# Optimization experiments

Hardware: AMD Instinct MI355X
Metric: run time of the kernel (lower is better)

## Reference

```python
import jax, jax.numpy as jnp
import numpy as np

D_MODEL = 1024
D_FF = 4 * D_MODEL
NUM_EXPERTS = 8
TOP_K = 2
B, L = 4, 2048


def setup_inputs() -> dict:
    key = jax.random.key(0)
    ks = jax.random.split(key, 7)
    s = 0.02
    return {
        "x": jax.random.normal(ks[0], (B, L, D_MODEL), dtype=jnp.float32),
        "Wr": jax.random.normal(ks[1], (D_MODEL, NUM_EXPERTS), dtype=jnp.float32) * s,
        "br": jnp.zeros((NUM_EXPERTS,), dtype=jnp.float32),
        "W1": jax.random.normal(ks[2], (NUM_EXPERTS, D_MODEL, D_FF), dtype=jnp.float32) * s,
        "b1": jnp.zeros((NUM_EXPERTS, D_FF), dtype=jnp.float32),
        "W2": jax.random.normal(ks[3], (NUM_EXPERTS, D_FF, D_MODEL), dtype=jnp.float32) * s,
        "b2": jnp.zeros((NUM_EXPERTS, D_MODEL), dtype=jnp.float32),
    }


def reference(x, Wr, br, W1, b1, W2, b2):
    Bb, Ll, D = x.shape
    x_flat = x.reshape(-1, D)                      # [T, D]
    T = x_flat.shape[0]

    # Router: softmax over experts, then top-k and renormalize (matches torch)
    logits = x_flat @ Wr + br                      # [T, E]
    probs = jax.nn.softmax(logits, axis=-1)
    topk_w, topk_idx = jax.lax.top_k(probs, TOP_K)  # [T, K]
    topk_w = topk_w / jnp.sum(topk_w, axis=-1, keepdims=True)

    # Per-token per-expert combine weights: w_full[t, e] = sum_k topk_w[t,k] * (topk_idx[t,k]==e)
    # (top_k indices are distinct, so scatter-add equals the masked-overwrite loop)
    w_full = jnp.zeros((T, NUM_EXPERTS), dtype=x.dtype)
    rows = jnp.arange(T)[:, None]
    w_full = w_full.at[rows, topk_idx].add(topk_w)

    # Dense all-expert MLP (same math as masked per-expert dispatch; dropout is eval/no-op)
    h = jax.nn.gelu(jnp.einsum("td,edf->etf", x_flat, W1) + b1[:, None, :], approximate=False)
    y = jnp.einsum("etf,efd->etd", h, W2) + b2[:, None, :]   # [E, T, D]
    out = jnp.einsum("te,etd->td", w_full, y)                # [T, D]
    return out.reshape(Bb, Ll, D)
```

## Files before the change

### kernel.cpp

```cpp
#include <hip/hip_runtime.h>
#include <hip/hip_bf16.h>

#define T_TOKENS 8192
#define DM 1024
#define DF 4096
#define NE 8
#define NROWS 16384

typedef __attribute__((ext_vector_type(8))) short bf16x8;
typedef __attribute__((ext_vector_type(8))) unsigned short ushort8;
typedef __attribute__((ext_vector_type(4))) float f32x4;

__device__ inline unsigned short f2bf(float f) {
  unsigned int u = __builtin_bit_cast(unsigned int, f);
  u = (u + 0x7fffu + ((u >> 16) & 1u)) >> 16;
  return (unsigned short)u;
}

__device__ inline float bf2f(unsigned short s) {
  unsigned int u = ((unsigned int)s) << 16;
  return __builtin_bit_cast(float, u);
}

__device__ __forceinline__ void gload16(const unsigned short* g, unsigned short* l) {
  __builtin_amdgcn_global_load_lds(
      (const __attribute__((address_space(1))) unsigned int*)g,
      (__attribute__((address_space(3))) unsigned int*)l,
      16, 0, 0);
}

__global__ void router_kernel(const float* __restrict__ x,
                              const float* __restrict__ Wr,
                              const float* __restrict__ br,
                              int* __restrict__ ctrl,
                              int* __restrict__ tope,
                              float* __restrict__ topw,
                              unsigned short* __restrict__ xb) {
  const int wid = threadIdx.x >> 6;
  const int lane = threadIdx.x & 63;
  const int t = blockIdx.x * 4 + wid;
  const float* xr = x + (size_t)t * DM;
  unsigned short* xbr = xb + (size_t)t * DM;
  float a[NE];
#pragma unroll
  for (int e = 0; e < NE; ++e) a[e] = 0.f;
#pragma unroll
  for (int it = 0; it < 4; ++it) {
    const int d0 = it * 256 + lane * 4;
    const float4 xv = *(const float4*)(xr + d0);
    ushort4 o;
    o.x = f2bf(xv.x); o.y = f2bf(xv.y); o.z = f2bf(xv.z); o.w = f2bf(xv.w);
    *(ushort4*)(xbr + d0) = o;
    const float xs[4] = {xv.x, xv.y, xv.z, xv.w};
#pragma unroll
    for (int j = 0; j < 4; ++j) {
      const float4 wa = *(const float4*)(Wr + (size_t)(d0 + j) * NE);
      const float4 wb = *(const float4*)(Wr + (size_t)(d0 + j) * NE + 4);
      a[0] += xs[j] * wa.x; a[1] += xs[j] * wa.y;
      a[2] += xs[j] * wa.z; a[3] += xs[j] * wa.w;
      a[4] += xs[j] * wb.x; a[5] += xs[j] * wb.y;
      a[6] += xs[j] * wb.z; a[7] += xs[j] * wb.w;
    }
  }
#pragma unroll
  for (int off = 32; off > 0; off >>= 1) {
#pragma unroll
    for (int e = 0; e < NE; ++e) a[e] += __shfl_xor(a[e], off);
  }
  if (lane == 0) {
    float lg[NE];
    float m = -1e30f;
#pragma unroll
    for (int e = 0; e < NE; ++e) { lg[e] = a[e] + br[e]; m = fmaxf(m, lg[e]); }
    float p[NE];
#pragma unroll
    for (int e = 0; e < NE; ++e) p[e] = expf(lg[e] - m);
    int i0 = 0;
#pragma unroll
    for (int e = 1; e < NE; ++e) if (p[e] > p[i0]) i0 = e;
    int i1 = (i0 == 0) ? 1 : 0;
#pragma unroll
    for (int e = 0; e < NE; ++e) if (e != i0 && p[e] > p[i1]) i1 = e;
    const float s = p[i0] + p[i1];
    tope[2 * t] = i0;
    tope[2 * t + 1] = i1;
    topw[2 * t] = p[i0] / s;
    topw[2 * t + 1] = p[i1] / s;
    atomicAdd(&ctrl[i0], 1);
    atomicAdd(&ctrl[i1], 1);
  }
}

__global__ void scan_kernel(int* __restrict__ ctrl) {
  if (threadIdx.x == 0 && blockIdx.x == 0) {
    int off = 0;
    for (int e = 0; e < NE; ++e) {
      ctrl[8 + e] = off;
      ctrl[20 + e] = off;
      off += ctrl[e];
    }
    ctrl[16] = off;
  }
}

__global__ void place_kernel(const int* __restrict__ tope,
                             const float* __restrict__ topw,
                             int* __restrict__ ctrl,
                             int* __restrict__ rowlist,
                             float* __restrict__ roww,
                             int* __restrict__ posmap) {
  const int t = blockIdx.x * blockDim.x + threadIdx.x;
#pragma unroll
  for (int k = 0; k < 2; ++k) {
    const int e = tope[2 * t + k];
    const int pos = atomicAdd(&ctrl[20 + e], 1);
    rowlist[pos] = t;
    roww[pos] = topw[2 * t + k];
    posmap[2 * t + k] = pos;
  }
}

__global__ void transpose_cvt_kernel(const float* __restrict__ in,
                                     unsigned short* __restrict__ outp,
                                     int R, int C) {
  __shared__ float tile[64][65];
  const int e = blockIdx.z;
  const int r0 = blockIdx.y * 64;
  const int c0 = blockIdx.x * 64;
  const float* src = in + ((size_t)e * R + r0) * C + c0;
  const int tid = threadIdx.x;
  const int rr0 = tid >> 4;
  const int cc4 = (tid & 15) * 4;
#pragma unroll
  for (int i = 0; i < 4; ++i) {
    const int rr = rr0 + i * 16;
    const float4 v = *(const float4*)(src + (size_t)rr * C + cc4);
    tile[rr][cc4] = v.x; tile[rr][cc4 + 1] = v.y;
    tile[rr][cc4 + 2] = v.z; tile[rr][cc4 + 3] = v.w;
  }
  __syncthreads();
  unsigned short* dst = outp + ((size_t)e * C + c0) * R + r0;
  const int orr = (tid & 7) * 8;
  const int oc0 = tid >> 3;
#pragma unroll
  for (int i = 0; i < 2; ++i) {
    const int oc = oc0 + i * 32;
    ushort8 o;
#pragma unroll
    for (int j = 0; j < 8; ++j) o[j] = f2bf(tile[orr + j][oc]);
    *(ushort8*)(dst + (size_t)oc * R + orr) = o;
  }
}

__global__ __launch_bounds__(256, 4) void gemm1_kernel(
    const unsigned short* __restrict__ xb,
    const unsigned short* __restrict__ w1t,
    const float* __restrict__ b1,
    const int* __restrict__ ctrl,
    const int* __restrict__ rowlist,
    unsigned short* __restrict__ h) {
  const int e = blockIdx.z;
  const int count = ctrl[e];
  const int mt = blockIdx.y;
  if (mt * 128 >= count) return;
  const int off = ctrl[8 + e];
  const int n0 = blockIdx.x * 128;
  const int tid = threadIdx.x;
  const int wid = tid >> 6;
  const int lane = tid & 63;
  const int wm = (wid & 1) * 64;
  const int wn = (wid >> 1) * 64;
  const int q = lane >> 4;
  const int l16 = lane & 15;
  const int rl = lane >> 3;
  const int ch = lane & 7;
  const int sch = ch ^ rl;

  __shared__ __attribute__((aligned(16))) unsigned short lA[128 * 64];
  __shared__ __attribute__((aligned(16))) unsigned short lB[128 * 64];

  const unsigned short* aBase[4];
  const unsigned short* bBase[4];
  unsigned short* lABase[4];
  unsigned short* lBBase[4];
#pragma unroll
  for (int i = 0; i < 4; ++i) {
    const int r = wid * 32 + i * 8 + rl;
    int rr = mt * 128 + r;
    if (rr >= count) rr = count - 1;
    const int tok = rowlist[off + rr];
    aBase[i] = xb + (size_t)tok * DM + sch * 8;
    bBase[i] = w1t + ((size_t)e * DF + n0 + r) * DM + sch * 8;
    lABase[i] = &lA[(wid * 32 + i * 8) * 64];
    lBBase[i] = &lB[(wid * 32 + i * 8) * 64];
  }

  f32x4 acc[4][4];
  const f32x4 z = {0.f, 0.f, 0.f, 0.f};
#pragma unroll
  for (int im = 0; im < 4; ++im)
#pragma unroll
    for (int in = 0; in < 4; ++in) acc[im][in] = z;

  for (int k0 = 0; k0 < DM; k0 += 64) {
#pragma unroll
    for (int i = 0; i < 4; ++i) gload16(aBase[i] + k0, lABase[i]);
#pragma unroll
    for (int i = 0; i < 4; ++i) gload16(bBase[i] + k0, lBBase[i]);
    __syncthreads();
#pragma unroll
    for (int ks = 0; ks < 2; ++ks) {
      const int pc = ((ks * 4 + q) ^ (l16 & 7)) * 8;
      bf16x8 af[4], bfr[4];
#pragma unroll
      for (int im = 0; im < 4; ++im)
        af[im] = *(const bf16x8*)&lA[(wm + im * 16 + l16) * 64 + pc];
#pragma unroll
      for (int in = 0; in < 4; ++in)
        bfr[in] = *(const bf16x8*)&lB[(wn + in * 16 + l16) * 64 + pc];
#pragma unroll
      for (int im = 0; im < 4; ++im)
#pragma unroll
        for (int in = 0; in < 4; ++in)
          acc[im][in] = __builtin_amdgcn_mfma_f32_16x16x32_bf16(
              bfr[in], af[im], acc[im][in], 0, 0, 0);
    }
    __syncthreads();
  }

#pragma unroll
  for (int im = 0; im < 4; ++im) {
    const int r = mt * 128 + wm + im * 16 + l16;
    if (r < count) {
      unsigned short* hrow = h + ((size_t)(off + r)) * DF + n0 + wn + q * 4;
#pragma unroll
      for (int in = 0; in < 4; ++in) {
        const float4 bv = *(const float4*)(b1 + (size_t)e * DF + n0 + wn + in * 16 + q * 4);
        float v0 = acc[im][in][0] + bv.x;
        float v1 = acc[im][in][1] + bv.y;
        float v2 = acc[im][in][2] + bv.z;
        float v3 = acc[im][in][3] + bv.w;
        ushort4 o;
        o.x = f2bf(0.5f * v0 * (1.0f + erff(v0 * 0.70710678118f)));
        o.y = f2bf(0.5f * v1 * (1.0f + erff(v1 * 0.70710678118f)));
        o.z = f2bf(0.5f * v2 * (1.0f + erff(v2 * 0.70710678118f)));
        o.w = f2bf(0.5f * v3 * (1.0f + erff(v3 * 0.70710678118f)));
        *(ushort4*)(hrow + in * 16) = o;
      }
    }
  }
}

__global__ __launch_bounds__(256, 2) void gemm2_kernel(
    const unsigned short* __restrict__ h,
    const unsigned short* __restrict__ w2t,
    const float* __restrict__ b2,
    const int* __restrict__ ctrl,
    unsigned short* __restrict__ y) {
  const int e = blockIdx.z;
  const int count = ctrl[e];
  const int mt = blockIdx.x;
  if (mt * 128 >= count) return;
  const int off = ctrl[8 + e];
  const int n0 = blockIdx.y * 256;
  const int tid = threadIdx.x;
  const int wid = tid >> 6;
  const int lane = tid & 63;
  const int wm = (wid & 1) * 64;
  const int wn = (wid >> 1) * 128;
  const int q = lane >> 4;
  const int l16 = lane & 15;
  const int rl = lane >> 3;
  const int ch = lane & 7;
  const int sch = ch ^ rl;

  __shared__ __attribute__((aligned(16))) unsigned short lA[128 * 64];
  __shared__ __attribute__((aligned(16))) unsigned short lB[256 * 64];

  const unsigned short* aBase[4];
  const unsigned short* bBase[8];
  unsigned short* lABase[4];
  unsigned short* lBBase[8];
#pragma unroll
  for (int i = 0; i < 4; ++i) {
    const int r = wid * 32 + i * 8 + rl;
    int rr = mt * 128 + r;
    if (rr >= count) rr = count - 1;
    aBase[i] = h + (size_t)(off + rr) * DF + sch * 8;
    lABase[i] = &lA[(wid * 32 + i * 8) * 64];
  }
#pragma unroll
  for (int i = 0; i < 8; ++i) {
    const int r = wid * 64 + i * 8 + rl;
    bBase[i] = w2t + ((size_t)e * DM + n0 + r) * DF + sch * 8;
    lBBase[i] = &lB[(wid * 64 + i * 8) * 64];
  }

  f32x4 acc[4][8];
  const f32x4 z = {0.f, 0.f, 0.f, 0.f};
#pragma unroll
  for (int im = 0; im < 4; ++im)
#pragma unroll
    for (int in = 0; in < 8; ++in) acc[im][in] = z;

  for (int k0 = 0; k0 < DF; k0 += 64) {
#pragma unroll
    for (int i = 0; i < 4; ++i) gload16(aBase[i] + k0, lABase[i]);
#pragma unroll
    for (int i = 0; i < 8; ++i) gload16(bBase[i] + k0, lBBase[i]);
    __syncthreads();
#pragma unroll
    for (int ks = 0; ks < 2; ++ks) {
      const int pc = ((ks * 4 + q) ^ (l16 & 7)) * 8;
      bf16x8 af[4], bfr[8];
#pragma unroll
      for (int im = 0; im < 4; ++im)
        af[im] = *(const bf16x8*)&lA[(wm + im * 16 + l16) * 64 + pc];
#pragma unroll
      for (int in = 0; in < 8; ++in)
        bfr[in] = *(const bf16x8*)&lB[(wn + in * 16 + l16) * 64 + pc];
#pragma unroll
      for (int im = 0; im < 4; ++im)
#pragma unroll
        for (int in = 0; in < 8; ++in)
          acc[im][in] = __builtin_amdgcn_mfma_f32_16x16x32_bf16(
              bfr[in], af[im], acc[im][in], 0, 0, 0);
    }
    __syncthreads();
  }

#pragma unroll
  for (int im = 0; im < 4; ++im) {
    const int r = mt * 128 + wm + im * 16 + l16;
    if (r < count) {
      unsigned short* yrow = y + ((size_t)(off + r)) * DM + n0 + wn + q * 4;
#pragma unroll
      for (int in = 0; in < 8; ++in) {
        const float4 bv = *(const float4*)(b2 + (size_t)e * DM + n0 + wn + in * 16 + q * 4);
        ushort4 o;
        o.x = f2bf(acc[im][in][0] + bv.x);
        o.y = f2bf(acc[im][in][1] + bv.y);
        o.z = f2bf(acc[im][in][2] + bv.z);
        o.w = f2bf(acc[im][in][3] + bv.w);
        *(ushort4*)(yrow + in * 16) = o;
      }
    }
  }
}

__global__ void combine_kernel(const unsigned short* __restrict__ y,
                               const int* __restrict__ posmap,
                               const float* __restrict__ topw,
                               float* __restrict__ out) {
  const int t = blockIdx.x;
  const int c = threadIdx.x * 4;
  const int p0 = posmap[2 * t];
  const int p1 = posmap[2 * t + 1];
  const float w0 = topw[2 * t];
  const float w1 = topw[2 * t + 1];
  const ushort4 a = *(const ushort4*)(y + (size_t)p0 * DM + c);
  const ushort4 b = *(const ushort4*)(y + (size_t)p1 * DM + c);
  float4 o;
  o.x = w0 * bf2f(a.x) + w1 * bf2f(b.x);
  o.y = w0 * bf2f(a.y) + w1 * bf2f(b.y);
  o.z = w0 * bf2f(a.z) + w1 * bf2f(b.z);
  o.w = w0 * bf2f(a.w) + w1 * bf2f(b.w);
  *(float4*)(out + (size_t)t * DM + c) = o;
}

extern "C" void kernel_launch(void* const* d_in, const int* in_sizes, int n_in,
                              void* d_out, int out_size, void* d_ws, size_t ws_size,
                              hipStream_t stream) {
  const float* x  = (const float*)d_in[0];
  const float* Wr = (const float*)d_in[1];
  const float* br = (const float*)d_in[2];
  const float* W1 = (const float*)d_in[3];
  const float* b1 = (const float*)d_in[4];
  const float* W2 = (const float*)d_in[5];
  const float* b2 = (const float*)d_in[6];
  float* out = (float*)d_out;

  char* p = (char*)d_ws;
  auto alloc = [&](size_t bytes) -> char* {
    char* r = p;
    p += (bytes + 255) & ~(size_t)255;
    return r;
  };
  int* ctrl = (int*)alloc(1024);
  int* tope = (int*)alloc((size_t)2 * T_TOKENS * 4);
  float* topw = (float*)alloc((size_t)2 * T_TOKENS * 4);
  int* rowlist = (int*)alloc((size_t)NROWS * 4);
  float* roww = (float*)alloc((size_t)NROWS * 4);
  int* posmap = (int*)alloc((size_t)NROWS * 4);
  unsigned short* xb  = (unsigned short*)alloc((size_t)T_TOKENS * DM * 2);
  unsigned short* w1t = (unsigned short*)alloc((size_t)NE * DF * DM * 2);
  unsigned short* w2t = (unsigned short*)alloc((size_t)NE * DM * DF * 2);
  unsigned short* h   = (unsigned short*)alloc((size_t)NROWS * DF * 2);
  if ((size_t)(p - (char*)d_ws) > ws_size) return;

  unsigned short* y = w1t;

  hipMemsetAsync(ctrl, 0, 1024, stream);

  router_kernel<<<T_TOKENS / 4, 256, 0, stream>>>(x, Wr, br, ctrl, tope, topw, xb);
  scan_kernel<<<1, 64, 0, stream>>>(ctrl);
  place_kernel<<<T_TOKENS / 256, 256, 0, stream>>>(tope, topw, ctrl, rowlist, roww, posmap);
  transpose_cvt_kernel<<<dim3(DF / 64, DM / 64, NE), 256, 0, stream>>>(W1, w1t, DM, DF);
  transpose_cvt_kernel<<<dim3(DM / 64, DF / 64, NE), 256, 0, stream>>>(W2, w2t, DF, DM);
  gemm1_kernel<<<dim3(DF / 128, 64, NE), 256, 0, stream>>>(xb, w1t, b1, ctrl, rowlist, h);
  gemm2_kernel<<<dim3(64, DM / 256, NE), 256, 0, stream>>>(h, w2t, b2, ctrl, y);
  combine_kernel<<<T_TOKENS, 256, 0, stream>>>(y, posmap, topw, out);
}
```

Baseline: 1.103 ms.

## Stage GEMM epilogues through LDS for coalesced stores; use fast erf approximation

Both GEMM epilogues now write the bf16 results into the reused shared-memory buffer with an XOR swizzle, then copy them out as full 16-byte contiguous row stores instead of scattered 8-byte fragment stores. GEMM1 also replaces erff with an Abramowitz-Stegun polynomial built on rcp and exp, and hoists the bias loads out of the row loop. This aims to cut epilogue store inefficiency and the cost of GELU, at the price of extra LDS traffic and barriers, plus a small accuracy loss in GELU.

```diff
diff --git a/kernel.cpp b/kernel.cpp
--- a/kernel.cpp
+++ b/kernel.cpp
@@ -20,6 +20,19 @@
 __device__ inline float bf2f(unsigned short s) {
   unsigned int u = ((unsigned int)s) << 16;
   return __builtin_bit_cast(float, u);
+}
+
+__device__ __forceinline__ float gelu_f(float v) {
+  const float z = fabsf(v) * 0.70710678118f;
+  const float t = __builtin_amdgcn_rcpf(1.0f + 0.3275911f * z);
+  const float poly =
+      t * (0.254829592f +
+           t * (-0.284496736f +
+                t * (1.421413741f + t * (-1.453152027f + t * 1.061405429f))));
+  const float ee = __expf(-z * z);
+  float er = 1.0f - poly * ee;
+  er = (v < 0.0f) ? -er : er;
+  return 0.5f * v * (1.0f + er);
 }
 
 __device__ __forceinline__ void gload16(const unsigned short* g, unsigned short* l) {
@@ -176,8 +189,9 @@
   const int ch = lane & 7;
   const int sch = ch ^ rl;
 
-  __shared__ __attribute__((aligned(16))) unsigned short lA[128 * 64];
-  __shared__ __attribute__((aligned(16))) unsigned short lB[128 * 64];
+  __shared__ __attribute__((aligned(16))) unsigned short smem[2 * 128 * 64];
+  unsigned short* lA = smem;
+  unsigned short* lB = smem + 128 * 64;
 
   const unsigned short* aBase[4];
   const unsigned short* bBase[4];
@@ -228,25 +242,35 @@
     __syncthreads();
   }
 
+  float4 bvv[4];
+#pragma unroll
+  for (int in = 0; in < 4; ++in)
+    bvv[in] = *(const float4*)(b1 + (size_t)e * DF + n0 + wn + in * 16 + q * 4);
 #pragma unroll
   for (int im = 0; im < 4; ++im) {
-    const int r = mt * 128 + wm + im * 16 + l16;
+    const int row = wm + im * 16 + l16;
+#pragma unroll
+    for (int in = 0; in < 4; ++in) {
+      const int col2 = (wn + in * 16 + q * 4) * 2;
+      ushort4 o;
+      o.x = f2bf(gelu_f(acc[im][in][0] + bvv[in].x));
+      o.y = f2bf(gelu_f(acc[im][in][1] + bvv[in].y));
+      o.z = f2bf(gelu_f(acc[im][in][2] + bvv[in].z));
+      o.w = f2bf(gelu_f(acc[im][in][3] + bvv[in].w));
+      *(ushort4*)((char*)smem + row * 256 + (col2 ^ ((row & 7) << 4))) = o;
+    }
+  }
+  __syncthreads();
+#pragma unroll
+  for (int i = 0; i < 8; ++i) {
+    const int flat = tid + i * 256;
+    const int row = flat >> 4;
+    const int c16 = (flat & 15) * 16;
+    const int r = mt * 128 + row;
     if (r < count) {
-      unsigned short* hrow = h + ((size_t)(off + r)) * DF + n0 + wn + q * 4;
-#pragma unroll
-      for (int in = 0; in < 4; ++in) {
-        const float4 bv = *(const float4*)(b1 + (size_t)e * DF + n0 + wn + in * 16 + q * 4);
-        float v0 = acc[im][in][0] + bv.x;
-        float v1 = acc[im][in][1] + bv.y;
-        float v2 = acc[im][in][2] + bv.z;
-        float v3 = acc[im][in][3] + bv.w;
-        ushort4 o;
-        o.x = f2bf(0.5f * v0 * (1.0f + erff(v0 * 0.70710678118f)));
-        o.y = f2bf(0.5f * v1 * (1.0f + erff(v1 * 0.70710678118f)));
-        o.z = f2bf(0.5f * v2 * (1.0f + erff(v2 * 0.70710678118f)));
-        o.w = f2bf(0.5f * v3 * (1.0f + erff(v3 * 0.70710678118f)));
-        *(ushort4*)(hrow + in * 16) = o;
-      }
+      const ushort8 v =
+          *(const ushort8*)((const char*)smem + row * 256 + (c16 ^ ((row & 7) << 4)));
+      *(ushort8*)(h + ((size_t)(off + r)) * DF + n0 + (c16 >> 1)) = v;
     }
   }
 }
@@ -274,8 +298,9 @@
   const int ch = lane & 7;
   const int sch = ch ^ rl;
 
-  __shared__ __attribute__((aligned(16))) unsigned short lA[128 * 64];
-  __shared__ __attribute__((aligned(16))) unsigned short lB[256 * 64];
+  __shared__ __attribute__((aligned(16))) unsigned short smem[128 * 64 + 256 * 64];
+  unsigned short* lA = smem;
+  unsigned short* lB = smem + 128 * 64;
 
   const unsigned short* aBase[4];
   const unsigned short* bBase[8];
@@ -329,22 +354,44 @@
     __syncthreads();
   }
 
-#pragma unroll
-  for (int im = 0; im < 4; ++im) {
-    const int r = mt * 128 + wm + im * 16 + l16;
-    if (r < count) {
-      unsigned short* yrow = y + ((size_t)(off + r)) * DM + n0 + wn + q * 4;
-#pragma unroll
-      for (int in = 0; in < 8; ++in) {
-        const float4 bv = *(const float4*)(b2 + (size_t)e * DM + n0 + wn + in * 16 + q * 4);
-        ushort4 o;
-        o.x = f2bf(acc[im][in][0] + bv.x);
-        o.y = f2bf(acc[im][in][1] + bv.y);
-        o.z = f2bf(acc[im][in][2] + bv.z);
-        o.w = f2bf(acc[im][in][3] + bv.w);
-        *(ushort4*)(yrow + in * 16) = o;
+  const int myhalf = wid >> 1;
+#pragma unroll
+  for (int p = 0; p < 2; ++p) {
+    if (myhalf == p) {
+      float4 bvv[8];
+#pragma unroll
+      for (int in = 0; in < 8; ++in)
+        bvv[in] =
+            *(const float4*)(b2 + (size_t)e * DM + n0 + p * 128 + in * 16 + q * 4);
+#pragma unroll
+      for (int im = 0; im < 4; ++im) {
+        const int row = wm + im * 16 + l16;
+#pragma unroll
+        for (int in = 0; in < 8; ++in) {
+          const int col2 = (in * 16 + q * 4) * 2;
+          ushort4 o;
+          o.x = f2bf(acc[im][in][0] + bvv[in].x);
+          o.y = f2bf(acc[im][in][1] + bvv[in].y);
+          o.z = f2bf(acc[im][in][2] + bvv[in].z);
+          o.w = f2bf(acc[im][in][3] + bvv[in].w);
+          *(ushort4*)((char*)smem + row * 256 + (col2 ^ ((row & 7) << 4))) = o;
+        }
       }
     }
+    __syncthreads();
+#pragma unroll
+    for (int i = 0; i < 8; ++i) {
+      const int flat = tid + i * 256;
+      const int row = flat >> 4;
+      const int c16 = (flat & 15) * 16;
+      const int r = mt * 128 + row;
+      if (r < count) {
+        const ushort8 v =
+            *(const ushort8*)((const char*)smem + row * 256 + (c16 ^ ((row & 7) << 4)));
+        *(ushort8*)(y + ((size_t)(off + r)) * DM + n0 + p * 128 + (c16 >> 1)) = v;
+      }
+    }
+    __syncthreads();
   }
 }
 
```

Result: slower. 1.176 ms (+6.6%).
